# Optimization experiments

Measured on AMD Instinct MI355X. Metric: run time of the kernel, lower is better.

The kernel has to match this reference:

```python
import jax, jax.numpy as jnp
import numpy as np

E = 1024      # emb_size == hidden_size
H = 8         # n_heads
BATCH = 8
NUM = 48      # table rows
KW = 48       # table columns (keys)
L = NUM * KW  # 2304


def _mha(q_in, kv_in, length, Wq, bq, Wk, bk, Wv, bv, Wo, bo, n_heads=H):
    # q_in: (B, T, E), kv_in: (B, S, E); returns (T, B, E) per the torch layout.
    B, T, Em = q_in.shape
    S = kv_in.shape[1]
    dh = Em // n_heads
    q = (q_in @ Wq + bq).reshape(B, T, n_heads, dh).transpose(0, 2, 1, 3)
    k = (kv_in @ Wk + bk).reshape(B, S, n_heads, dh).transpose(0, 2, 1, 3)
    v = (kv_in @ Wv + bv).reshape(B, S, n_heads, dh).transpose(0, 2, 1, 3)
    scores = jnp.einsum('bhtd,bhsd->bhts', q, k) / jnp.asarray(np.sqrt(dh), q.dtype)
    mask = jnp.arange(S) < length  # memory_lengths masking
    scores = jnp.where(mask[None, None, None, :], scores, jnp.finfo(scores.dtype).min)
    attn = jax.nn.softmax(scores, axis=-1)
    out = jnp.einsum('bhts,bhsd->bhtd', attn, v).transpose(0, 2, 1, 3).reshape(B, T, Em)
    out = out @ Wo + bo
    return out.transpose(1, 0, 2)  # (T, B, E)


def setup_inputs() -> dict:
    key = jax.random.key(0)
    ks = jax.random.split(key, 24)

    def W(k, shape, s=0.03):
        return jax.random.normal(k, shape, dtype=jnp.float32) * s

    inp = {
        'emb': jax.random.normal(ks[0], (L, BATCH, E), dtype=jnp.float32),
        # col attention params
        'Wq_c': W(ks[1], (E, E)), 'bq_c': jnp.zeros((E,), jnp.float32),
        'Wk_c': W(ks[2], (E, E)), 'bk_c': jnp.zeros((E,), jnp.float32),
        'Wv_c': W(ks[3], (E, E)), 'bv_c': jnp.zeros((E,), jnp.float32),
        'Wo_c': W(ks[4], (E, E)), 'bo_c': jnp.zeros((E,), jnp.float32),
        # row attention params
        'Wq_r': W(ks[5], (E, E)), 'bq_r': jnp.zeros((E,), jnp.float32),
        'Wk_r': W(ks[6], (E, E)), 'bk_r': jnp.zeros((E,), jnp.float32),
        'Wv_r': W(ks[7], (E, E)), 'bv_r': jnp.zeros((E,), jnp.float32),
        'Wo_r': W(ks[8], (E, E)), 'bo_r': jnp.zeros((E,), jnp.float32),
        # fusion layers
        'W_gen': W(ks[9], (2 * E, E)),
        'W_mlp1': W(ks[10], (2 * E, E)),
        'W_mlp2': W(ks[11], (E, 1)),
        # scalar forward args
        'start_id': 0, 'end_id': L - 1,
        'num': NUM, 'num_tensor': NUM,
        'kw_num': KW, 'kw_num_tensor': KW,
        'batch': BATCH,
    }
    return inp


def reference(emb, Wq_c, bq_c, Wk_c, bk_c, Wv_c, bv_c, Wo_c, bo_c,
              Wq_r, bq_r, Wk_r, bk_r, Wv_r, bv_r, Wo_r, bo_r,
              W_gen, W_mlp1, W_mlp2,
              start_id, end_id, num, num_tensor, kw_num, kw_num_tensor, batch):
    Em = emb.shape[-1]
    length = end_id - start_id + 1  # = num * kw_num
    # emb.narrow(0, start_id, length): (L, batch, E)
    rep = emb[start_id:start_id + length]
    # -> (kw_num, batch*num, E)
    home_ply_rep = rep.transpose(1, 0, 2).reshape(batch * num, kw_num, Em).transpose(1, 0, 2)

    # --- column-dim encoding: attention over the `num` (row) axis ---
    col_mb = jnp.swapaxes(home_ply_rep.reshape(kw_num, batch, num, Em), 0, 2)  # (num, batch, kw, E)
    col_mb = col_mb.reshape(num, batch * kw_num, Em)
    col_q = col_mb.transpose(1, 0, 2)  # (batch*kw, num, E)
    col_rep = _mha(col_q, col_q, num_tensor, Wq_c, bq_c, Wk_c, bk_c, Wv_c, bv_c, Wo_c, bo_c)
    # (num, batch*kw, E) -> (kw_num, batch*num, E)
    col_dim_rep = jnp.swapaxes(col_rep.reshape(num, batch, kw_num, Em), 0, 2).reshape(kw_num, batch * num, Em)

    # --- row-dim encoding: attention over the `kw_num` (column) axis ---
    row_q = col_dim_rep.transpose(1, 0, 2)  # (batch*num, kw, E)
    row_dim_rep = _mha(row_q, row_q, kw_num_tensor, Wq_r, bq_r, Wk_r, bk_r, Wv_r, bv_r, Wo_r, bo_r)  # (kw, b*n, E)

    # --- fusion: concat + Linear + tanh, MLP scores, softmax over {row, col} ---
    gen_rep = jnp.tanh(jnp.concatenate([row_dim_rep, col_dim_rep], axis=-1) @ W_gen)

    def mlp_score(x):
        return jnp.tanh(jnp.concatenate([x, gen_rep], axis=-1) @ W_mlp1) @ W_mlp2  # (kw, b*n, 1)

    row_score = mlp_score(row_dim_rep)
    col_score = mlp_score(col_dim_rep)
    w = jax.nn.softmax(jnp.concatenate([row_score, col_score], axis=-1), axis=-1)  # (kw, b*n, 2)
    home_ply_memory_bank = w[..., 0:1] * row_dim_rep + w[..., 1:2] * col_dim_rep
    # no_fusion=True -> residual add
    home_ply_memory_bank = home_ply_memory_bank + home_ply_rep

    row_for_ptr = row_dim_rep.reshape(kw_num, batch, num, Em)
    col_for_ptr = col_dim_rep.reshape(kw_num, batch, num, Em)

    # row_aggregation == 'mean'
    home_ply_row_rep = home_ply_memory_bank.mean(axis=0)  # (batch*num, E)
    home_ply_row_rep = home_ply_row_rep.reshape(batch, num, Em).transpose(1, 0, 2)  # (num, batch, E)
    return (home_ply_row_rep, home_ply_memory_bank, col_for_ptr, row_for_ptr)
```

## Files before the change

kernel.cpp:

```cpp
#include <hip/hip_runtime.h>
#include <hip/hip_bf16.h>
#include <stdint.h>

typedef unsigned short u16;
typedef unsigned int   u32;
typedef __attribute__((ext_vector_type(4))) float f32x4;
typedef __attribute__((ext_vector_type(2))) float f32x2;
typedef __attribute__((ext_vector_type(8))) short s16x8;

#define DEV __device__ __forceinline__

static constexpr int EDIM  = 1024;
static constexpr int MROWS = 8 * 48 * 48;
static constexpr int MT    = MROWS / 128;

DEV float b2f(u16 x) { u32 u = ((u32)x) << 16; float f; __builtin_memcpy(&f, &u, 4); return f; }
DEV u16 f2b(float f) {
    u32 u; __builtin_memcpy(&u, &f, 4);
    u32 r = (u + 0x7FFFu + ((u >> 16) & 1u)) >> 16;
    return (u16)r;
}

#define GLDS16(gsrc, ldst) __builtin_amdgcn_global_load_lds( \
    (const __attribute__((address_space(1))) u32*)(gsrc),    \
    (__attribute__((address_space(3))) u32*)(ldst), 16, 0, 0)

__global__ void wconv_kernel(const float* __restrict__ W, u16* __restrict__ Wt,
                             int K, int N) {
    __shared__ u16 tile[64][65];
    int n0 = blockIdx.x * 64, k0 = blockIdx.y * 64;
    int tx = threadIdx.x & 63, ty = threadIdx.x >> 6;
#pragma unroll
    for (int i = 0; i < 16; ++i) {
        int r = ty * 16 + i;
        tile[r][tx] = f2b(W[(size_t)(k0 + r) * N + n0 + tx]);
    }
    __syncthreads();
#pragma unroll
    for (int i = 0; i < 16; ++i) {
        int r = ty * 16 + i;
        Wt[(size_t)(n0 + r) * K + k0 + tx] = tile[tx][r];
    }
}

__global__ void bconcat_kernel(const float* __restrict__ a, const float* __restrict__ b,
                               const float* __restrict__ c, float* __restrict__ out) {
    int i = blockIdx.x * 256 + threadIdx.x;
    out[i] = (i < 1024) ? a[i] : ((i < 2048) ? b[i - 1024] : c[i - 2048]);
}

__global__ void gather_kernel(const float* __restrict__ emb, u16* __restrict__ Xc) {
    int gid = blockIdx.x * 256 + threadIdx.x;
    int r = gid >> 9, c2 = gid & 511;
    int b = r / 2304, k = (r / 48) % 48, n = r % 48;
    int src = (n * 48 + k) * 8 + b;
    f32x2 v = *(const f32x2*)&emb[(size_t)src * EDIM + c2 * 2];
    u32 p = (u32)f2b(v.x) | ((u32)f2b(v.y) << 16);
    *(u32*)&Xc[(size_t)r * EDIM + c2 * 2] = p;
}

__global__ void zero_kernel(float* __restrict__ p, int n) {
    int i = blockIdx.x * 256 + threadIdx.x;
    if (i < n) p[i] = 0.f;
}

template<int KTOT, bool DUALA, bool TANH, bool PERM, bool SCORE, bool WRC, int OMAP>
__global__ __launch_bounds__(256, 4) void gemm_kernel(
    const u16* __restrict__ A1, const u16* __restrict__ A2, int lda,
    const u16* __restrict__ Bt, const float* __restrict__ bias,
    u16* __restrict__ C, int ldc, float* __restrict__ outF,
    const float* __restrict__ w2, float* __restrict__ score) {
    __shared__ u16 lA[2][128 * 32];
    __shared__ u16 lB[2][128 * 32];
    int bid = blockIdx.x;
    int mt = bid % MT, nt = bid / MT;
    int m0 = mt * 128, n0 = nt * 128;
    int tid = threadIdx.x, lane = tid & 63, wv = tid >> 6;
    int wm = wv >> 1, wn = wv & 1;
    int fr = lane & 15, qq = lane >> 4, fk = qq * 8;

    f32x4 acc[4][4];
#pragma unroll
    for (int i = 0; i < 4; ++i)
#pragma unroll
        for (int j = 0; j < 4; ++j) acc[i][j] = (f32x4)0.f;

    auto STAGE = [&](int bsel, int kt) {
        int k0 = kt * 32;
        const u16* As = A1; int ka = k0;
        if (DUALA && k0 >= 1024) { As = A2; ka = k0 - 1024; }
#pragma unroll
        for (int i = 0; i < 2; ++i) {
            int c = wv * 2 + i;
            int r = c * 16 + (lane >> 2);
            int qg = ((lane & 3) - (r >> 1)) & 3;
            GLDS16(As + (size_t)(m0 + r) * lda + ka + qg * 8, &lA[bsel][c * 512]);
            GLDS16(Bt + (size_t)(n0 + r) * KTOT + k0 + qg * 8, &lB[bsel][c * 512]);
        }
    };

    constexpr int NT = KTOT / 32;
    STAGE(0, 0);
    for (int kt = 0; kt < NT; ++kt) {
        __syncthreads();
        if (kt + 1 < NT) STAGE((kt + 1) & 1, kt + 1);
        const u16* la = &lA[kt & 1][0];
        const u16* lb = &lB[kt & 1][0];
        s16x8 af[4], bf[4];
#pragma unroll
        for (int mf = 0; mf < 4; ++mf) {
            int rr = wm * 64 + mf * 16 + fr;
            af[mf] = *(const s16x8*)&la[rr * 32 + (((qq + (rr >> 1)) & 3) * 8)];
        }
#pragma unroll
        for (int nf = 0; nf < 4; ++nf) {
            int rn = wn * 64 + nf * 16 + fr;
            bf[nf] = *(const s16x8*)&lb[rn * 32 + (((qq + (rn >> 1)) & 3) * 8)];
        }
#pragma unroll
        for (int mf = 0; mf < 4; ++mf)
#pragma unroll
            for (int nf = 0; nf < 4; ++nf)
                acc[mf][nf] = __builtin_amdgcn_mfma_f32_16x16x32_bf16(af[mf], bf[nf], acc[mf][nf], 0, 0, 0);
    }

    int crow4 = qq * 4;
#pragma unroll
    for (int mf = 0; mf < 4; ++mf) {
#pragma unroll
        for (int j = 0; j < 4; ++j) {
            int row = m0 + wm * 64 + mf * 16 + crow4 + j;
            int orow = row;
            int o32 = 0;
            if (PERM || OMAP == 1) {
                int b = row / 2304, k = (row / 48) % 48, n = row % 48;
                if (PERM) orow = (b * 48 + n) * 48 + k;
                if (OMAP == 1) o32 = k * 384 + b * 48 + n;
            }
            if (OMAP == 2) {
                int b = row / 2304, n = (row / 48) % 48, k = row % 48;
                o32 = k * 384 + b * 48 + n;
            }
            float sc_part = 0.f;
#pragma unroll
            for (int nf = 0; nf < 4; ++nf) {
                int col = n0 + wn * 64 + nf * 16 + fr;
                float v = acc[mf][nf][j];
                if (bias) v += bias[col];
                if (TANH) v = tanhf(v);
                if (WRC) C[(size_t)orow * ldc + col] = f2b(v);
                if (OMAP) outF[(size_t)o32 * EDIM + col] = v;
                if (SCORE) sc_part += v * w2[col];
            }
            if (SCORE) {
                sc_part += __shfl_xor(sc_part, 1);
                sc_part += __shfl_xor(sc_part, 2);
                sc_part += __shfl_xor(sc_part, 4);
                sc_part += __shfl_xor(sc_part, 8);
                if (fr == 0) atomicAdd(&score[row], sc_part);
            }
        }
    }
}

__global__ __launch_bounds__(64) void attn_kernel(u16* __restrict__ QKV) {
    __shared__ u16 lVt[128 * 72];
    __shared__ u16 lP[48 * 72];
    const int LDQ = 3072;
    int bb = blockIdx.x >> 3, h = blockIdx.x & 7;
    int lane = threadIdx.x;
    u16* Qp = QKV + (size_t)bb * 48 * LDQ + h * 128;
    const u16* Kp = Qp + 1024;
    const u16* Vp = Qp + 2048;

#pragma unroll
    for (int i = 0; i < 48; ++i) {
        u32 vv = *(const u32*)&Vp[(size_t)i * LDQ + lane * 2];
        lVt[(lane * 2) * 72 + i]     = (u16)(vv & 0xffffu);
        lVt[(lane * 2 + 1) * 72 + i] = (u16)(vv >> 16);
    }
    for (int i = lane; i < 128 * 16; i += 64) { int d = i >> 4, c = 48 + (i & 15); lVt[d * 72 + c] = 0; }
    for (int i = lane; i < 48 * 16; i += 64)  { int t = i >> 4, c = 48 + (i & 15); lP[t * 72 + c] = 0; }
    __syncthreads();

    int fr = lane & 15, fk = (lane >> 4) * 8, crow4 = (lane >> 4) * 4;
    f32x4 sc[3][3];
#pragma unroll
    for (int mf = 0; mf < 3; ++mf)
#pragma unroll
        for (int nf = 0; nf < 3; ++nf) sc[mf][nf] = (f32x4)0.f;

#pragma unroll
    for (int kk = 0; kk < 4; ++kk) {
        s16x8 aq[3], bk[3];
#pragma unroll
        for (int mf = 0; mf < 3; ++mf) aq[mf] = *(const s16x8*)&Qp[(size_t)(mf * 16 + fr) * LDQ + kk * 32 + fk];
#pragma unroll
        for (int nf = 0; nf < 3; ++nf) bk[nf] = *(const s16x8*)&Kp[(size_t)(nf * 16 + fr) * LDQ + kk * 32 + fk];
#pragma unroll
        for (int mf = 0; mf < 3; ++mf)
#pragma unroll
            for (int nf = 0; nf < 3; ++nf)
                sc[mf][nf] = __builtin_amdgcn_mfma_f32_16x16x32_bf16(aq[mf], bk[nf], sc[mf][nf], 0, 0, 0);
    }

    const float scale = 0.08838834764831845f;
#pragma unroll
    for (int mf = 0; mf < 3; ++mf) {
#pragma unroll
        for (int j = 0; j < 4; ++j) {
            float v0 = sc[mf][0][j] * scale;
            float v1 = sc[mf][1][j] * scale;
            float v2 = sc[mf][2][j] * scale;
            float mx = fmaxf(v0, fmaxf(v1, v2));
            mx = fmaxf(mx, __shfl_xor(mx, 1));
            mx = fmaxf(mx, __shfl_xor(mx, 2));
            mx = fmaxf(mx, __shfl_xor(mx, 4));
            mx = fmaxf(mx, __shfl_xor(mx, 8));
            float e0 = __expf(v0 - mx), e1 = __expf(v1 - mx), e2 = __expf(v2 - mx);
            float s = e0 + e1 + e2;
            s += __shfl_xor(s, 1);
            s += __shfl_xor(s, 2);
            s += __shfl_xor(s, 4);
            s += __shfl_xor(s, 8);
            float inv = 1.f / s;
            int t = mf * 16 + crow4 + j;
            lP[t * 72 + 0  + fr] = f2b(e0 * inv);
            lP[t * 72 + 16 + fr] = f2b(e1 * inv);
            lP[t * 72 + 32 + fr] = f2b(e2 * inv);
        }
    }
    __syncthreads();

    f32x4 o[3][8];
#pragma unroll
    for (int mf = 0; mf < 3; ++mf)
#pragma unroll
        for (int nf = 0; nf < 8; ++nf) o[mf][nf] = (f32x4)0.f;

#pragma unroll
    for (int kk = 0; kk < 2; ++kk) {
        s16x8 ap[3];
#pragma unroll
        for (int mf = 0; mf < 3; ++mf) ap[mf] = *(const s16x8*)&lP[(mf * 16 + fr) * 72 + kk * 32 + fk];
#pragma unroll
        for (int nf = 0; nf < 8; ++nf) {
            s16x8 bv = *(const s16x8*)&lVt[(nf * 16 + fr) * 72 + kk * 32 + fk];
#pragma unroll
            for (int mf = 0; mf < 3; ++mf)
                o[mf][nf] = __builtin_amdgcn_mfma_f32_16x16x32_bf16(ap[mf], bv, o[mf][nf], 0, 0, 0);
        }
    }
#pragma unroll
    for (int mf = 0; mf < 3; ++mf)
#pragma unroll
        for (int nf = 0; nf < 8; ++nf)
#pragma unroll
            for (int j = 0; j < 4; ++j) {
                int t = mf * 16 + crow4 + j, d = nf * 16 + fr;
                Qp[(size_t)t * LDQ + d] = f2b(o[mf][nf][j]);
            }
}

__global__ void combine_kernel(const u16* __restrict__ RDR, const u16* __restrict__ CDR,
                               const float* __restrict__ srow, const float* __restrict__ scol,
                               const float* __restrict__ emb, float* __restrict__ out_mb) {
    int o = blockIdx.x;
    int k = o / 384, b = (o / 48) & 7, n = o % 48;
    int r2 = (b * 48 + n) * 48 + k;
    float rs = srow[r2], cs = scol[r2];
    float m = fmaxf(rs, cs);
    float e0 = __expf(rs - m), e1 = __expf(cs - m);
    float inv = 1.f / (e0 + e1);
    float w0 = e0 * inv, w1 = e1 * inv;
    const size_t rb = (size_t)r2 * EDIM;
    const size_t ob = (size_t)o * EDIM;
    const size_t eb = ((size_t)(n * 48 + k) * 8 + b) * EDIM;
    for (int e = threadIdx.x; e < EDIM; e += 256) {
        float rv = b2f(RDR[rb + e]);
        float cv = b2f(CDR[rb + e]);
        out_mb[ob + e] = w0 * rv + w1 * cv + emb[eb + e];
    }
}

__global__ void mean_kernel(const float* __restrict__ mb, float* __restrict__ out0) {
    int idx = blockIdx.x * 256 + threadIdx.x;
    int n = idx >> 13, b = (idx >> 10) & 7, e = idx & 1023;
    float s = 0.f;
#pragma unroll 8
    for (int k = 0; k < 48; ++k) s += mb[((size_t)(k * 384 + b * 48 + n)) * EDIM + e];
    out0[idx] = s * (1.f / 48.f);
}

extern "C" void kernel_launch(void* const* d_in, const int* in_sizes, int n_in,
                              void* d_out, int out_size, void* d_ws, size_t ws_size,
                              hipStream_t stream) {
    const float* emb    = (const float*)d_in[0];
    const float* Wq_c   = (const float*)d_in[1];
    const float* bq_c   = (const float*)d_in[2];
    const float* Wk_c   = (const float*)d_in[3];
    const float* bk_c   = (const float*)d_in[4];
    const float* Wv_c   = (const float*)d_in[5];
    const float* bv_c   = (const float*)d_in[6];
    const float* Wo_c   = (const float*)d_in[7];
    const float* bo_c   = (const float*)d_in[8];
    const float* Wq_r   = (const float*)d_in[9];
    const float* bq_r   = (const float*)d_in[10];
    const float* Wk_r   = (const float*)d_in[11];
    const float* bk_r   = (const float*)d_in[12];
    const float* Wv_r   = (const float*)d_in[13];
    const float* bv_r   = (const float*)d_in[14];
    const float* Wo_r   = (const float*)d_in[15];
    const float* bo_r   = (const float*)d_in[16];
    const float* W_gen  = (const float*)d_in[17];
    const float* W_mlp1 = (const float*)d_in[18];
    const float* W_mlp2 = (const float*)d_in[19];

    char* ws = (char*)d_ws;
    size_t off = 0;
    auto alloc = [&](size_t bytes) { char* p = ws + off; off += (bytes + 255) & ~(size_t)255; return p; };
    u16*   WqkvC = (u16*)alloc((size_t)3072 * 1024 * 2);
    u16*   WqkvR = (u16*)alloc((size_t)3072 * 1024 * 2);
    u16*   WoC   = (u16*)alloc((size_t)1024 * 1024 * 2);
    u16*   WoR   = (u16*)alloc((size_t)1024 * 1024 * 2);
    u16*   WgT   = (u16*)alloc((size_t)1024 * 2048 * 2);
    u16*   W1T   = (u16*)alloc((size_t)1024 * 2048 * 2);
    float* bqkvC = (float*)alloc(3072 * 4);
    float* bqkvR = (float*)alloc(3072 * 4);
    u16*   XA    = (u16*)alloc((size_t)MROWS * 1024 * 2);
    u16*   QKV   = (u16*)alloc((size_t)MROWS * 3072 * 2);
    u16*   CDR   = (u16*)alloc((size_t)MROWS * 1024 * 2);
    u16*   RDR   = (u16*)alloc((size_t)MROWS * 1024 * 2);
    float* score_row = (float*)alloc((size_t)MROWS * 4);
    float* score_col = (float*)alloc((size_t)MROWS * 4);
    (void)ws_size; (void)in_sizes; (void)n_in; (void)out_size;

    dim3 tb(256);
    wconv_kernel<<<dim3(16, 16), tb, 0, stream>>>(Wq_c, WqkvC,                   1024, 1024);
    wconv_kernel<<<dim3(16, 16), tb, 0, stream>>>(Wk_c, WqkvC + 1024 * 1024,     1024, 1024);
    wconv_kernel<<<dim3(16, 16), tb, 0, stream>>>(Wv_c, WqkvC + 2 * 1024 * 1024, 1024, 1024);
    wconv_kernel<<<dim3(16, 16), tb, 0, stream>>>(Wo_c, WoC,                     1024, 1024);
    wconv_kernel<<<dim3(16, 16), tb, 0, stream>>>(Wq_r, WqkvR,                   1024, 1024);
    wconv_kernel<<<dim3(16, 16), tb, 0, stream>>>(Wk_r, WqkvR + 1024 * 1024,     1024, 1024);
    wconv_kernel<<<dim3(16, 16), tb, 0, stream>>>(Wv_r, WqkvR + 2 * 1024 * 1024, 1024, 1024);
    wconv_kernel<<<dim3(16, 16), tb, 0, stream>>>(Wo_r, WoR,                     1024, 1024);
    wconv_kernel<<<dim3(16, 32), tb, 0, stream>>>(W_gen,  WgT, 2048, 1024);
    wconv_kernel<<<dim3(16, 32), tb, 0, stream>>>(W_mlp1, W1T, 2048, 1024);
    bconcat_kernel<<<12, tb, 0, stream>>>(bq_c, bk_c, bv_c, bqkvC);
    bconcat_kernel<<<12, tb, 0, stream>>>(bq_r, bk_r, bv_r, bqkvR);

    gather_kernel<<<MROWS * 512 / 256, tb, 0, stream>>>(emb, XA);
    zero_kernel<<<(2 * MROWS + 255) / 256, tb, 0, stream>>>(score_row, 2 * MROWS);

    float* out = (float*)d_out;
    float* out_mb  = out + 393216;
    float* out_col = out + 393216 + 18874368;
    float* out_row = out + 393216 + 2 * 18874368;

    const int G8 = MT * 8, G24 = MT * 24;
    gemm_kernel<1024, false, false, false, false, true, 0><<<G24, tb, 0, stream>>>(
        XA, nullptr, 1024, WqkvC, bqkvC, QKV, 3072, nullptr, nullptr, nullptr);
    attn_kernel<<<384 * 8, 64, 0, stream>>>(QKV);
    gemm_kernel<1024, false, false, true, false, true, 1><<<G8, tb, 0, stream>>>(
        QKV, nullptr, 3072, WoC, bo_c, CDR, 1024, out_col, nullptr, nullptr);
    gemm_kernel<1024, false, false, false, false, true, 0><<<G24, tb, 0, stream>>>(
        CDR, nullptr, 1024, WqkvR, bqkvR, QKV, 3072, nullptr, nullptr, nullptr);
    attn_kernel<<<384 * 8, 64, 0, stream>>>(QKV);
    gemm_kernel<1024, false, false, false, false, true, 2><<<G8, tb, 0, stream>>>(
        QKV, nullptr, 3072, WoR, bo_r, RDR, 1024, out_row, nullptr, nullptr);
    gemm_kernel<2048, true, true, false, false, true, 0><<<G8, tb, 0, stream>>>(
        RDR, CDR, 1024, WgT, nullptr, XA, 1024, nullptr, nullptr, nullptr);
    gemm_kernel<2048, true, true, false, true, false, 0><<<G8, tb, 0, stream>>>(
        RDR, XA, 1024, W1T, nullptr, nullptr, 1024, nullptr, W_mlp2, score_row);
    gemm_kernel<2048, true, true, false, true, false, 0><<<G8, tb, 0, stream>>>(
        CDR, XA, 1024, W1T, nullptr, nullptr, 1024, nullptr, W_mlp2, score_col);

    combine_kernel<<<MROWS, tb, 0, stream>>>(RDR, CDR, score_row, score_col, emb, out_mb);
    mean_kernel<<<393216 / 256, tb, 0, stream>>>(out_mb, out);
}
```

Before: 1.079 ms.

## Replace 128x128 GEMM with 256x256 tile, 8-wave ping-pong pipelined kernel

```diff
diff --git a/kernel.cpp b/kernel.cpp
--- a/kernel.cpp
+++ b/kernel.cpp
@@ -12,7 +12,7 @@
 
 static constexpr int EDIM  = 1024;
 static constexpr int MROWS = 8 * 48 * 48;
-static constexpr int MT    = MROWS / 128;
+static constexpr int MT256 = MROWS / 256;
 
 DEV float b2f(u16 x) { u32 u = ((u32)x) << 16; float f; __builtin_memcpy(&f, &u, 4); return f; }
 DEV u16 f2b(float f) {
@@ -24,6 +24,9 @@
 #define GLDS16(gsrc, ldst) __builtin_amdgcn_global_load_lds( \
     (const __attribute__((address_space(1))) u32*)(gsrc),    \
     (__attribute__((address_space(3))) u32*)(ldst), 16, 0, 0)
+
+#define BAR()   __builtin_amdgcn_s_barrier()
+#define LGKM0() asm volatile("s_waitcnt lgkmcnt(0)" ::: "memory")
 
 __global__ void wconv_kernel(const float* __restrict__ W, u16* __restrict__ Wt,
                              int K, int N) {
@@ -64,72 +67,181 @@
     if (i < n) p[i] = 0.f;
 }
 
+DEV s16x8 ldsrd(const u16* lds, int r, int kk, int qq) {
+    return *(const s16x8*)&lds[r * 64 + kk * 32 + (((qq + (r >> 1)) & 3) << 3)];
+}
+
+DEV void stage_tileA(u16* lds, const u16* Ag, int lda, int m0, int ka,
+                     int h, int wv, int lane) {
+#pragma unroll
+    for (int i = 0; i < 2; ++i) {
+        int blk  = wv * 2 + i;
+        int row0 = (h + 2 * (blk >> 3)) * 64 + (blk & 7) * 8;
+        int rr   = row0 + (lane >> 3);
+        int pg   = lane & 7;
+        int qq   = ((pg & 3) - (rr >> 1)) & 3;
+        const u16* g = Ag + (size_t)(m0 + rr) * lda + ka + (pg >> 2) * 32 + qq * 8;
+        GLDS16(g, lds + row0 * 64);
+    }
+}
+
+DEV void stage_tileB(u16* lds, const u16* Bg, int ldb, int n0, int kb,
+                     int h, int wv, int lane) {
+#pragma unroll
+    for (int i = 0; i < 2; ++i) {
+        int blk  = wv * 2 + i;
+        int row0 = (blk >> 2) * 64 + h * 32 + (blk & 3) * 8;
+        int rr   = row0 + (lane >> 3);
+        int pg   = lane & 7;
+        int qq   = ((pg & 3) - (rr >> 1)) & 3;
+        const u16* g = Bg + (size_t)(n0 + rr) * ldb + kb + (pg >> 2) * 32 + qq * 8;
+        GLDS16(g, lds + row0 * 64);
+    }
+}
+
 template<int KTOT, bool DUALA, bool TANH, bool PERM, bool SCORE, bool WRC, int OMAP>
-__global__ __launch_bounds__(256, 4) void gemm_kernel(
+__global__ __launch_bounds__(512, 2) void gemm256_kernel(
     const u16* __restrict__ A1, const u16* __restrict__ A2, int lda,
     const u16* __restrict__ Bt, const float* __restrict__ bias,
     u16* __restrict__ C, int ldc, float* __restrict__ outF,
     const float* __restrict__ w2, float* __restrict__ score) {
-    __shared__ u16 lA[2][128 * 32];
-    __shared__ u16 lB[2][128 * 32];
+    __shared__ u16 lA[2][256 * 64];
+    __shared__ u16 lB[2][256 * 64];
+    constexpr int NT = KTOT / 64;
+
     int bid = blockIdx.x;
-    int mt = bid % MT, nt = bid / MT;
-    int m0 = mt * 128, n0 = nt * 128;
+    int mt = bid % MT256, nt = bid / MT256;
+    int m0 = mt * 256, n0 = nt * 256;
     int tid = threadIdx.x, lane = tid & 63, wv = tid >> 6;
-    int wm = wv >> 1, wn = wv & 1;
-    int fr = lane & 15, qq = lane >> 4, fk = qq * 8;
-
-    f32x4 acc[4][4];
-#pragma unroll
-    for (int i = 0; i < 4; ++i)
+    int wm = wv >> 2, wn = wv & 3;
+    int fr = lane & 15, qq = lane >> 4;
+
+    auto Asel = [&](int ts, const u16*& Ag, int& ka) {
+        ka = ts * 64; Ag = A1;
+        if (DUALA && ka >= 1024) { Ag = A2; ka -= 1024; }
+    };
+
+    f32x4 acc[8][4];
+#pragma unroll
+    for (int i = 0; i < 8; ++i)
 #pragma unroll
         for (int j = 0; j < 4; ++j) acc[i][j] = (f32x4)0.f;
 
-    auto STAGE = [&](int bsel, int kt) {
-        int k0 = kt * 32;
-        const u16* As = A1; int ka = k0;
-        if (DUALA && k0 >= 1024) { As = A2; ka = k0 - 1024; }
-#pragma unroll
-        for (int i = 0; i < 2; ++i) {
-            int c = wv * 2 + i;
-            int r = c * 16 + (lane >> 2);
-            int qg = ((lane & 3) - (r >> 1)) & 3;
-            GLDS16(As + (size_t)(m0 + r) * lda + ka + qg * 8, &lA[bsel][c * 512]);
-            GLDS16(Bt + (size_t)(n0 + r) * KTOT + k0 + qg * 8, &lB[bsel][c * 512]);
+    {
+        const u16* Ag; int ka; Asel(0, Ag, ka);
+        stage_tileA(&lA[0][0], Ag, lda, m0, ka, 0, wv, lane);
+        stage_tileA(&lA[0][0], Ag, lda, m0, ka, 1, wv, lane);
+        stage_tileB(&lB[0][0], Bt, KTOT, n0, 0, 0, wv, lane);
+        stage_tileB(&lB[0][0], Bt, KTOT, n0, 0, 1, wv, lane);
+    }
+    if (NT > 1) {
+        const u16* Ag; int ka; Asel(1, Ag, ka);
+        stage_tileA(&lA[1][0], Ag, lda, m0, ka, 0, wv, lane);
+        stage_tileB(&lB[1][0], Bt, KTOT, n0, 64, 0, wv, lane);
+        stage_tileB(&lB[1][0], Bt, KTOT, n0, 64, 1, wv, lane);
+    }
+    asm volatile("s_waitcnt vmcnt(6)" ::: "memory");
+    BAR();
+
+    s16x8 A8[8], B0[4], B1[4];
+
+    for (int t = 0; t < NT; ++t) {
+        int buf = t & 1;
+        const u16* lAb = &lA[buf][0];
+        const u16* lBb = &lB[buf][0];
+
+#pragma unroll
+        for (int m = 0; m < 4; ++m)
+#pragma unroll
+            for (int kk = 0; kk < 2; ++kk)
+                A8[m * 2 + kk] = ldsrd(lAb, wm * 128 + m * 16 + fr, kk, qq);
+#pragma unroll
+        for (int n = 0; n < 2; ++n)
+#pragma unroll
+            for (int kk = 0; kk < 2; ++kk)
+                B0[n * 2 + kk] = ldsrd(lBb, wn * 64 + n * 16 + fr, kk, qq);
+        if (t + 1 < NT) {
+            const u16* Ag; int ka; Asel(t + 1, Ag, ka);
+            stage_tileA(&lA[buf ^ 1][0], Ag, lda, m0, ka, 1, wv, lane);
         }
-    };
-
-    constexpr int NT = KTOT / 32;
-    STAGE(0, 0);
-    for (int kt = 0; kt < NT; ++kt) {
-        __syncthreads();
-        if (kt + 1 < NT) STAGE((kt + 1) & 1, kt + 1);
-        const u16* la = &lA[kt & 1][0];
-        const u16* lb = &lB[kt & 1][0];
-        s16x8 af[4], bf[4];
-#pragma unroll
-        for (int mf = 0; mf < 4; ++mf) {
-            int rr = wm * 64 + mf * 16 + fr;
-            af[mf] = *(const s16x8*)&la[rr * 32 + (((qq + (rr >> 1)) & 3) * 8)];
+        BAR(); LGKM0();
+        __builtin_amdgcn_s_setprio(1);
+#pragma unroll
+        for (int m = 0; m < 4; ++m)
+#pragma unroll
+            for (int n = 0; n < 2; ++n)
+#pragma unroll
+                for (int kk = 0; kk < 2; ++kk)
+                    acc[m][n] = __builtin_amdgcn_mfma_f32_16x16x32_bf16(
+                        A8[m * 2 + kk], B0[n * 2 + kk], acc[m][n], 0, 0, 0);
+        __builtin_amdgcn_s_setprio(0);
+        BAR();
+
+#pragma unroll
+        for (int n = 0; n < 2; ++n)
+#pragma unroll
+            for (int kk = 0; kk < 2; ++kk)
+                B1[n * 2 + kk] = ldsrd(lBb, wn * 64 + 32 + n * 16 + fr, kk, qq);
+        if (t + 2 < NT) {
+            const u16* Ag; int ka; Asel(t + 2, Ag, ka);
+            stage_tileA(&lA[buf][0], Ag, lda, m0, ka, 0, wv, lane);
         }
-#pragma unroll
-        for (int nf = 0; nf < 4; ++nf) {
-            int rn = wn * 64 + nf * 16 + fr;
-            bf[nf] = *(const s16x8*)&lb[rn * 32 + (((qq + (rn >> 1)) & 3) * 8)];
-        }
-#pragma unroll
-        for (int mf = 0; mf < 4; ++mf)
-#pragma unroll
-            for (int nf = 0; nf < 4; ++nf)
-                acc[mf][nf] = __builtin_amdgcn_mfma_f32_16x16x32_bf16(af[mf], bf[nf], acc[mf][nf], 0, 0, 0);
+        BAR(); LGKM0();
+        __builtin_amdgcn_s_setprio(1);
+#pragma unroll
+        for (int m = 0; m < 4; ++m)
+#pragma unroll
+            for (int n = 0; n < 2; ++n)
+#pragma unroll
+                for (int kk = 0; kk < 2; ++kk)
+                    acc[m][n + 2] = __builtin_amdgcn_mfma_f32_16x16x32_bf16(
+                        A8[m * 2 + kk], B1[n * 2 + kk], acc[m][n + 2], 0, 0, 0);
+        __builtin_amdgcn_s_setprio(0);
+        BAR();
+
+#pragma unroll
+        for (int m = 0; m < 4; ++m)
+#pragma unroll
+            for (int kk = 0; kk < 2; ++kk)
+                A8[m * 2 + kk] = ldsrd(lAb, wm * 128 + 64 + m * 16 + fr, kk, qq);
+        if (t + 2 < NT)
+            stage_tileB(&lB[buf][0], Bt, KTOT, n0, (t + 2) * 64, 0, wv, lane);
+        BAR(); LGKM0();
+        __builtin_amdgcn_s_setprio(1);
+#pragma unroll
+        for (int m = 0; m < 4; ++m)
+#pragma unroll
+            for (int n = 0; n < 2; ++n)
+#pragma unroll
+                for (int kk = 0; kk < 2; ++kk)
+                    acc[m + 4][n] = __builtin_amdgcn_mfma_f32_16x16x32_bf16(
+                        A8[m * 2 + kk], B0[n * 2 + kk], acc[m + 4][n], 0, 0, 0);
+        __builtin_amdgcn_s_setprio(0);
+        BAR();
+
+        if (t + 2 < NT)
+            stage_tileB(&lB[buf][0], Bt, KTOT, n0, (t + 2) * 64, 1, wv, lane);
+        __builtin_amdgcn_s_setprio(1);
+#pragma unroll
+        for (int m = 0; m < 4; ++m)
+#pragma unroll
+            for (int n = 0; n < 2; ++n)
+#pragma unroll
+                for (int kk = 0; kk < 2; ++kk)
+                    acc[m + 4][n + 2] = __builtin_amdgcn_mfma_f32_16x16x32_bf16(
+                        A8[m * 2 + kk], B1[n * 2 + kk], acc[m + 4][n + 2], 0, 0, 0);
+        __builtin_amdgcn_s_setprio(0);
+        if (t < NT - 2)       asm volatile("s_waitcnt vmcnt(6)" ::: "memory");
+        else if (t == NT - 2) asm volatile("s_waitcnt vmcnt(0)" ::: "memory");
+        BAR();
     }
 
     int crow4 = qq * 4;
 #pragma unroll
-    for (int mf = 0; mf < 4; ++mf) {
+    for (int mf = 0; mf < 8; ++mf) {
 #pragma unroll
         for (int j = 0; j < 4; ++j) {
-            int row = m0 + wm * 64 + mf * 16 + crow4 + j;
+            int row = m0 + wm * 128 + mf * 16 + crow4 + j;
             int orow = row;
             int o32 = 0;
             if (PERM || OMAP == 1) {
@@ -357,22 +469,23 @@
     float* out_col = out + 393216 + 18874368;
     float* out_row = out + 393216 + 2 * 18874368;
 
-    const int G8 = MT * 8, G24 = MT * 24;
-    gemm_kernel<1024, false, false, false, false, true, 0><<<G24, tb, 0, stream>>>(
+    dim3 tb512(512);
+    const int G12 = MT256 * 12, G4 = MT256 * 4;
+    gemm256_kernel<1024, false, false, false, false, true, 0><<<G12, tb512, 0, stream>>>(
         XA, nullptr, 1024, WqkvC, bqkvC, QKV, 3072, nullptr, nullptr, nullptr);
     attn_kernel<<<384 * 8, 64, 0, stream>>>(QKV);
-    gemm_kernel<1024, false, false, true, false, true, 1><<<G8, tb, 0, stream>>>(
+    gemm256_kernel<1024, false, false, true, false, true, 1><<<G4, tb512, 0, stream>>>(
         QKV, nullptr, 3072, WoC, bo_c, CDR, 1024, out_col, nullptr, nullptr);
-    gemm_kernel<1024, false, false, false, false, true, 0><<<G24, tb, 0, stream>>>(
+    gemm256_kernel<1024, false, false, false, false, true, 0><<<G12, tb512, 0, stream>>>(
         CDR, nullptr, 1024, WqkvR, bqkvR, QKV, 3072, nullptr, nullptr, nullptr);
     attn_kernel<<<384 * 8, 64, 0, stream>>>(QKV);
-    gemm_kernel<1024, false, false, false, false, true, 2><<<G8, tb, 0, stream>>>(
+    gemm256_kernel<1024, false, false, false, false, true, 2><<<G4, tb512, 0, stream>>>(
         QKV, nullptr, 3072, WoR, bo_r, RDR, 1024, out_row, nullptr, nullptr);
-    gemm_kernel<2048, true, true, false, false, true, 0><<<G8, tb, 0, stream>>>(
+    gemm256_kernel<2048, true, true, false, false, true, 0><<<G4, tb512, 0, stream>>>(
         RDR, CDR, 1024, WgT, nullptr, XA, 1024, nullptr, nullptr, nullptr);
-    gemm_kernel<2048, true, true, false, true, false, 0><<<G8, tb, 0, stream>>>(
+    gemm256_kernel<2048, true, true, false, true, false, 0><<<G4, tb512, 0, stream>>>(
         RDR, XA, 1024, W1T, nullptr, nullptr, 1024, nullptr, W_mlp2, score_row);
-    gemm_kernel<2048, true, true, false, true, false, 0><<<G8, tb, 0, stream>>>(
+    gemm256_kernel<2048, true, true, false, true, false, 0><<<G4, tb512, 0, stream>>>(
         CDR, XA, 1024, W1T, nullptr, nullptr, 1024, nullptr, W_mlp2, score_col);
 
     combine_kernel<<<MROWS, tb, 0, stream>>>(RDR, CDR, score_row, score_col, emb, out_mb);
```

New measurement: 1.363 ms. 26.4% more time.
